# Kernel tuning notes

Measured on AMD Instinct MI355X. Metric: run time of the kernel, lower is better.

## Reference

```python
import jax, jax.numpy as jnp
import numpy as np

B, T, I, H = 128, 800, 300, 32  # batch, sl, input dim, hidden


def setup_inputs() -> dict:
    key = jax.random.key(0)
    ks = jax.random.split(key, 10)
    s_h = 1.0 / np.sqrt(H)
    s_t = 1.0 / np.sqrt(T)
    s_f = 1.0 / np.sqrt(H * T)
    u = lambda k, shape, s: jax.random.uniform(k, shape, jnp.float32, -s, s)
    return {
        "x": jax.random.normal(ks[0], (B, T, I), jnp.float32),
        "W_ih": u(ks[1], (4 * H, I), s_h),   # torch gate order: i, f, g, o
        "W_hh": u(ks[2], (4 * H, H), s_h),
        "b_ih": u(ks[3], (4 * H,), s_h),
        "b_hh": u(ks[4], (4 * H,), s_h),
        "Ww": u(ks[5], (T, T), s_t),         # Linear(sl, sl)
        "bw": u(ks[6], (T,), s_t),
        "Wfc": u(ks[7], (1, H * T), s_f),    # Linear(h*sl, 1)
        "bfc": u(ks[8], (1,), s_f),
    }


def _lstm(x, W_ih, W_hh, b_ih, b_hh):
    # Precompute input projections for all timesteps: [B, T, 4H]
    gx = jnp.einsum('bti,gi->btg', x, W_ih) + b_ih + b_hh
    h0 = jnp.zeros((x.shape[0], H), x.dtype)
    c0 = jnp.zeros_like(h0)

    def step(carry, g_t):
        h, c = carry
        g = g_t + h @ W_hh.T  # [B, 4H]
        i_g, f_g, g_g, o_g = jnp.split(g, 4, axis=-1)
        i_g = jax.nn.sigmoid(i_g)
        f_g = jax.nn.sigmoid(f_g)
        g_g = jnp.tanh(g_g)
        o_g = jax.nn.sigmoid(o_g)
        c = f_g * c + i_g * g_g
        h = o_g * jnp.tanh(c)
        return (h, c), h

    _, hs = jax.lax.scan(step, (h0, c0), jnp.swapaxes(gx, 0, 1))  # hs: [T, B, H]
    return jnp.swapaxes(hs, 0, 1)  # [B, T, H]


def reference(x, W_ih, W_hh, b_ih, b_hh, Ww, bw, Wfc, bfc):
    out = _lstm(x, W_ih, W_hh, b_ih, b_hh)  # [B, T, H]
    # permute -> Linear(sl, sl) over the seq axis -> permute back, fused in one einsum
    # q[b, s, h] = sum_t out[b, t, h] * Ww[s, t] + bw[s]
    q = jnp.einsum('bth,st->bsh', out, Ww) + bw[None, :, None]
    qk = out * q  # [B, T, H]
    out_fc = qk.reshape(qk.shape[0], -1) @ Wfc.T + bfc  # [B, 1]
    return (out_fc, qk)
```

## Files before the change

kernel.cpp:

```cpp
#include <hip/hip_runtime.h>
#include <stdint.h>

#define B_SZ 128
#define T_SZ 800
#define I_SZ 300
#define KPAD 320
#define H_SZ 32
#define G_SZ 128
#define NWIN 50
#define NBUF 4
#define TP   808
#define NTILE 50
#define NGRP 13

typedef float f32x4 __attribute__((ext_vector_type(4)));
typedef _Float16 half8 __attribute__((ext_vector_type(8)));
typedef _Float16 half2v __attribute__((ext_vector_type(2)));

union FragH { half8 v; _Float16 h[8]; uint4 u4; };
union PkU  { uint u; _Float16 h[2]; };
union HsU  { ushort s; _Float16 h; };
union Pk2  { uint u; half2v v; };

#if __has_builtin(__builtin_amdgcn_permlane32_swap)
#define HAVE_PL32 1
#else
#define HAVE_PL32 0
#endif

#if __has_builtin(__builtin_amdgcn_fdot2) && __has_builtin(__builtin_amdgcn_mov_dpp)
#define HAVE_DOT2 1
#else
#define HAVE_DOT2 0
#endif

__device__ __forceinline__ float tanhfast(float x) {
    float ax = fabsf(x);
    float z = __expf(-2.f * ax);
    float r = __fdividef(1.f - z, 1.f + z);
    return __builtin_copysignf(r, x);
}
__device__ __forceinline__ float sigmoidf_(float x) {
    return __fdividef(1.f, 1.f + __expf(-x));
}
__device__ __forceinline__ float bcast_lane(float v, int srclane) {
    return __int_as_float(__builtin_amdgcn_readlane(__float_as_int(v), srclane));
}

__global__ __launch_bounds__(256) void k_prep(
    const float* __restrict__ W_ih, const float* __restrict__ Ww,
    _Float16* __restrict__ W_ihH, _Float16* __restrict__ WwH)
{
    int i = blockIdx.x * 256 + threadIdx.x;
    if (i < G_SZ * KPAD) {
        int r = i / KPAD, k = i - r * KPAD;
        W_ihH[i] = (k < I_SZ) ? (_Float16)W_ih[r * I_SZ + k] : (_Float16)0.f;
    }
    int j = i - G_SZ * KPAD;
    if (j >= 0 && j < T_SZ * T_SZ) WwH[j] = (_Float16)Ww[j];
}

__global__ __launch_bounds__(256) void k_main(
    const float* __restrict__ x, const _Float16* __restrict__ W_ihH,
    const float* __restrict__ W_hh,
    const float* __restrict__ b_ih, const float* __restrict__ b_hh,
    const float* __restrict__ bfc,
    _Float16* __restrict__ histG,
    float* __restrict__ out)
{
    const int b    = blockIdx.x;
    const int tid  = threadIdx.x;
    const int wave = tid >> 6;
    const int lane = tid & 63;
    const int m16  = lane & 15;
    const int quad = lane >> 4;

    __shared__ __align__(16) ushort hist[H_SZ][TP];
    __shared__ __align__(16) uint   gxbuf[NBUF][16][64];
    __shared__ int produced, consumed;

    if (tid == 0) { produced = 0; consumed = 0; out[b] = bfc[0]; }
    __syncthreads();

    if (wave == 0) {
#if HAVE_PL32
        bool pl_pick_x;
        {
            auto t2 = __builtin_amdgcn_permlane32_swap(lane, lane, false, false);
            pl_pick_x = ((int)__builtin_amdgcn_readlane((int)t2[0], 63) < (int)H_SZ);
        }
#endif
        float c = 0.f;

#if HAVE_DOT2 && HAVE_PL32
        uint WpA[16], WpB[16];
#pragma unroll
        for (int j = 0; j < 16; ++j) {
            HsU a0_, a1_, b0_, b1_;
            a0_.h = (_Float16)W_hh[lane * H_SZ + 2*j];
            a1_.h = (_Float16)W_hh[lane * H_SZ + 2*j + 1];
            b0_.h = (_Float16)W_hh[(lane + 64) * H_SZ + 2*j];
            b1_.h = (_Float16)W_hh[(lane + 64) * H_SZ + 2*j + 1];
            WpA[j] = (uint)a0_.s | ((uint)a1_.s << 16);
            WpB[j] = (uint)b0_.s | ((uint)b1_.s << 16);
        }
        int hpk = 0;

        for (int w = 0; w < NWIN; ++w) {
            while (__atomic_load_n(&produced, __ATOMIC_ACQUIRE) < w + 1)
                __builtin_amdgcn_s_sleep(2);
#pragma unroll 4
            for (int tl = 0; tl < 16; ++tl) {
                const int t = w * 16 + tl;
                PkU g; g.u = gxbuf[w & (NBUF - 1)][tl][lane];
                float aA0 = 0.f, aA1 = 0.f, aB0 = 0.f, aB1 = 0.f;
#pragma unroll
                for (int j = 0; j < 16; j += 2) {
                    Pk2 h0; h0.u = (uint)__builtin_amdgcn_readlane(hpk, 32 + 2*j);
                    Pk2 h1; h1.u = (uint)__builtin_amdgcn_readlane(hpk, 32 + 2*j + 2);
                    Pk2 wa0; wa0.u = WpA[j];     Pk2 wb0; wb0.u = WpB[j];
                    Pk2 wa1; wa1.u = WpA[j + 1]; Pk2 wb1; wb1.u = WpB[j + 1];
                    aA0 = __builtin_amdgcn_fdot2(wa0.v, h0.v, aA0, false);
                    aB0 = __builtin_amdgcn_fdot2(wb0.v, h0.v, aB0, false);
                    aA1 = __builtin_amdgcn_fdot2(wa1.v, h1.v, aA1, false);
                    aB1 = __builtin_amdgcn_fdot2(wb1.v, h1.v, aB1, false);
                }
                float g0 = (aA0 + aA1) + (float)g.h[0];
                float g1 = (aB0 + aB1) + (float)g.h[1];

                float a0 = sigmoidf_(g0);
                float zz = (lane < H_SZ) ? g1 : 0.5f * g1;
                float th = tanhfast(zz);
                float a1 = (lane < H_SZ) ? th : 0.5f * th + 0.5f;

                float ig  = a0 * a1;
                auto rr = __builtin_amdgcn_permlane32_swap(
                    __float_as_int(ig), __float_as_int(ig), false, false);
                float igs = __int_as_float(pl_pick_x ? (int)rr[0] : (int)rr[1]);
                c = a0 * c + igs;
                float h = a1 * tanhfast(c);

                HsU hc; hc.h = (_Float16)h;
                uint hcu = (uint)hc.s;
                uint hnb = (uint)__builtin_amdgcn_mov_dpp((int)hcu, 0xB1, 0xF, 0xF, false);
                hpk = (int)((hnb << 16) | hcu);
                if (lane >= H_SZ)
                    hist[lane - H_SZ][t] = hc.s;
            }
            __atomic_store_n(&consumed, w + 1, __ATOMIC_RELEASE);
        }
#else
        float W0[H_SZ], W1[H_SZ];
#pragma unroll
        for (int k = 0; k < H_SZ; ++k) W0[k] = W_hh[lane * H_SZ + k];
#pragma unroll
        for (int k = 0; k < H_SZ; ++k) W1[k] = W_hh[(lane + 64) * H_SZ + k];
        float hprev = 0.f;

        for (int w = 0; w < NWIN; ++w) {
            while (__atomic_load_n(&produced, __ATOMIC_ACQUIRE) < w + 1)
                __builtin_amdgcn_s_sleep(2);
#pragma unroll 4
            for (int tl = 0; tl < 16; ++tl) {
                const int t = w * 16 + tl;
                PkU g; g.u = gxbuf[w & (NBUF - 1)][tl][lane];
                float p0=0.f,p1=0.f,p2=0.f,p3=0.f;
                float q0=0.f,q1=0.f,q2=0.f,q3=0.f;
#pragma unroll
                for (int k = 0; k < H_SZ; k += 4) {
                    float h0 = bcast_lane(hprev, H_SZ + k + 0);
                    float h1 = bcast_lane(hprev, H_SZ + k + 1);
                    float h2 = bcast_lane(hprev, H_SZ + k + 2);
                    float h3 = bcast_lane(hprev, H_SZ + k + 3);
                    p0 += W0[k+0]*h0; q0 += W1[k+0]*h0;
                    p1 += W0[k+1]*h1; q1 += W1[k+1]*h1;
                    p2 += W0[k+2]*h2; q2 += W1[k+2]*h2;
                    p3 += W0[k+3]*h3; q3 += W1[k+3]*h3;
                }
                float g0 = ((p0 + p1) + (p2 + p3)) + (float)g.h[0];
                float g1 = ((q0 + q1) + (q2 + q3)) + (float)g.h[1];

                float a0 = sigmoidf_(g0);
                float zz = (lane < H_SZ) ? g1 : 0.5f * g1;
                float th = tanhfast(zz);
                float a1 = (lane < H_SZ) ? th : 0.5f * th + 0.5f;

                float ig  = a0 * a1;
                float igs = __shfl_up(ig, 32, 64);
                c = a0 * c + igs;
                float h = a1 * tanhfast(c);
                hprev = h;
                if (lane >= H_SZ) {
                    HsU hs; hs.h = (_Float16)h;
                    hist[lane - H_SZ][t] = hs.s;
                }
            }
            __atomic_store_n(&consumed, w + 1, __ATOMIC_RELEASE);
        }
#endif
    } else {
        float bias[8];
#pragma unroll
        for (int nt = 0; nt < 8; ++nt)
            bias[nt] = b_ih[nt * 16 + m16] + b_hh[nt * 16 + m16];
        const float* xb = x + (size_t)b * T_SZ * I_SZ;

        for (int w = wave - 1; w < NWIN; w += 3) {
            const float* xrow = xb + (size_t)(w * 16 + m16) * I_SZ;
            f32x4 acc[8];
#pragma unroll
            for (int nt = 0; nt < 8; ++nt) acc[nt] = (f32x4){0.f, 0.f, 0.f, 0.f};

            for (int ks = 0; ks < 9; ++ks) {
                const int k0 = ks * 32 + quad * 8;
                f32x4 x0 = *(const f32x4*)(xrow + k0);
                f32x4 x1 = *(const f32x4*)(xrow + k0 + 4);
                FragH a;
                a.h[0] = (_Float16)x0[0]; a.h[1] = (_Float16)x0[1];
                a.h[2] = (_Float16)x0[2]; a.h[3] = (_Float16)x0[3];
                a.h[4] = (_Float16)x1[0]; a.h[5] = (_Float16)x1[1];
                a.h[6] = (_Float16)x1[2]; a.h[7] = (_Float16)x1[3];
#pragma unroll
                for (int nt = 0; nt < 8; ++nt) {
                    FragH bb;
                    bb.u4 = *(const uint4*)(W_ihH + (size_t)(nt * 16 + m16) * KPAD + k0);
                    acc[nt] = __builtin_amdgcn_mfma_f32_16x16x32_f16(a.v, bb.v, acc[nt], 0, 0, 0);
                }
            }
            {
                FragH a;
#pragma unroll
                for (int jj = 0; jj < 8; ++jj) {
                    int k = 288 + quad * 8 + jj;
                    a.h[jj] = (k < I_SZ) ? (_Float16)xrow[k] : (_Float16)0.f;
                }
#pragma unroll
                for (int nt = 0; nt < 8; ++nt) {
                    FragH bb;
                    bb.u4 = *(const uint4*)(W_ihH + (size_t)(nt * 16 + m16) * KPAD + 288 + quad * 8);
                    acc[nt] = __builtin_amdgcn_mfma_f32_16x16x32_f16(a.v, bb.v, acc[nt], 0, 0, 0);
                }
            }
            while (__atomic_load_n(&consumed, __ATOMIC_ACQUIRE) < w - (NBUF - 1))
                __builtin_amdgcn_s_sleep(8);
#pragma unroll
            for (int nt = 0; nt < 4; ++nt)
#pragma unroll
                for (int r = 0; r < 4; ++r) {
                    PkU p;
                    p.h[0] = (_Float16)(acc[nt][r]     + bias[nt]);
                    p.h[1] = (_Float16)(acc[nt + 4][r] + bias[nt + 4]);
                    gxbuf[w & (NBUF - 1)][quad * 4 + r][nt * 16 + m16] = p.u;
                }
            while (__atomic_load_n(&produced, __ATOMIC_ACQUIRE) != w)
                __builtin_amdgcn_s_sleep(8);
            __atomic_store_n(&produced, w + 1, __ATOMIC_RELEASE);
        }
    }

    __syncthreads();
    _Float16* hGb = histG + (size_t)b * H_SZ * T_SZ;
    for (int i = tid; i < H_SZ * (T_SZ / 8); i += 256) {
        int r = i / (T_SZ / 8), cc = i - r * (T_SZ / 8);
        *(uint4*)(hGb + (size_t)r * T_SZ + cc * 8) = *(const uint4*)&hist[r][cc * 8];
    }
}

__global__ __launch_bounds__(256) void k_attn(
    const _Float16* __restrict__ histG, const _Float16* __restrict__ WwH,
    const float* __restrict__ bw, const float* __restrict__ Wfc,
    float* __restrict__ out)
{
    const int b    = blockIdx.x;
    const int grp  = blockIdx.y;
    const int tid  = threadIdx.x;
    const int wave = tid >> 6;
    const int lane = tid & 63;
    const int m16  = lane & 15;
    const int quad = lane >> 4;

    __shared__ __align__(16) ushort histL[H_SZ][TP];

    const _Float16* hb = histG + (size_t)b * H_SZ * T_SZ;
    for (int i = tid; i < H_SZ * (T_SZ / 8); i += 256) {
        int r = i / (T_SZ / 8), c = i - r * (T_SZ / 8);
        *(uint4*)&histL[r][c * 8] = *(const uint4*)(hb + (size_t)r * T_SZ + c * 8);
    }
    __syncthreads();

    const int st = grp * 4 + wave;
    if (st >= NTILE) return;
    const int s0 = st * 16;

    float* region = out + B_SZ + (size_t)b * T_SZ * H_SZ;
    f32x4 acc0 = (f32x4){0.f,0.f,0.f,0.f};
    f32x4 acc1 = (f32x4){0.f,0.f,0.f,0.f};
    const _Float16* wwrow = WwH + (size_t)(s0 + m16) * T_SZ;

#pragma unroll 2
    for (int t0 = 0; t0 < T_SZ; t0 += 32) {
        FragH a, b0, b1;
        a.u4  = *(const uint4*)(wwrow + t0 + quad * 8);
        b0.u4 = *(const uint4*)&histL[m16][t0 + quad * 8];
        b1.u4 = *(const uint4*)&histL[16 + m16][t0 + quad * 8];
        acc0 = __builtin_amdgcn_mfma_f32_16x16x32_f16(a.v, b0.v, acc0, 0, 0, 0);
        acc1 = __builtin_amdgcn_mfma_f32_16x16x32_f16(a.v, b1.v, acc1, 0, 0, 0);
    }

    float fc_acc = 0.f;
#pragma unroll
    for (int r = 0; r < 4; ++r) {
        int s = s0 + quad * 4 + r;
        float bws = bw[s];
        HsU u0; u0.s = histL[m16][s];      float h0 = (float)u0.h;
        HsU u1; u1.s = histL[16 + m16][s]; float h1 = (float)u1.h;
        float q0 = acc0[r] + bws;
        float q1 = acc1[r] + bws;
        float qk0 = h0 * q0;
        float qk1 = h1 * q1;
        region[(size_t)s * H_SZ + m16]      = qk0;
        region[(size_t)s * H_SZ + 16 + m16] = qk1;
        fc_acc += qk0 * Wfc[s * H_SZ + m16];
        fc_acc += qk1 * Wfc[s * H_SZ + 16 + m16];
    }

#pragma unroll
    for (int off = 32; off > 0; off >>= 1)
        fc_acc += __shfl_down(fc_acc, off, 64);
    if (lane == 0) atomicAdd(out + b, fc_acc);
}

extern "C" void kernel_launch(void* const* d_in, const int* in_sizes, int n_in,
                              void* d_out, int out_size, void* d_ws, size_t ws_size,
                              hipStream_t stream) {
    const float* x    = (const float*)d_in[0];
    const float* W_ih = (const float*)d_in[1];
    const float* W_hh = (const float*)d_in[2];
    const float* b_ih = (const float*)d_in[3];
    const float* b_hh = (const float*)d_in[4];
    const float* Ww   = (const float*)d_in[5];
    const float* bw   = (const float*)d_in[6];
    const float* Wfc  = (const float*)d_in[7];
    const float* bfc  = (const float*)d_in[8];

    float* out = (float*)d_out;

    _Float16* W_ihH = (_Float16*)d_ws;
    _Float16* WwH   = (_Float16*)((char*)d_ws + (size_t)G_SZ * KPAD * 2);
    _Float16* histG = (_Float16*)((char*)d_ws + (size_t)G_SZ * KPAD * 2
                                             + (size_t)T_SZ * T_SZ * 2);

    int prep_n = G_SZ * KPAD + T_SZ * T_SZ;
    k_prep<<<(prep_n + 255) / 256, 256, 0, stream>>>(W_ih, Ww, W_ihH, WwH);
    k_main<<<B_SZ, 256, 0, stream>>>(x, W_ihH, W_hh, b_ih, b_hh, bfc, histG, out);
    k_attn<<<dim3(B_SZ, NGRP), 256, 0, stream>>>(histG, WwH, bw, Wfc, out);
}
```

Before: 397.1 us.

## Process two batch elements per block to interleave independent LSTM recurrences

Each k_main block now handles two batch elements, running both LSTM recurrences interleaved in the single recurrence wave and computing input projections for both in the producer waves. The intent is to hide the latency of the serial per-timestep dependency chain (dot products, lane broadcasts, activations) by giving the scheduler two independent chains. The grid is halved, so fewer CUs are used and per-block work and shared memory roughly double.

```diff
diff --git a/kernel.cpp b/kernel.cpp
--- a/kernel.cpp
+++ b/kernel.cpp
@@ -68,18 +68,20 @@
     _Float16* __restrict__ histG,
     float* __restrict__ out)
 {
-    const int b    = blockIdx.x;
+    const int bA   = blockIdx.x * 2;
+    const int bB   = bA + 1;
     const int tid  = threadIdx.x;
     const int wave = tid >> 6;
     const int lane = tid & 63;
     const int m16  = lane & 15;
     const int quad = lane >> 4;
 
-    __shared__ __align__(16) ushort hist[H_SZ][TP];
-    __shared__ __align__(16) uint   gxbuf[NBUF][16][64];
+    __shared__ __align__(16) ushort histA[H_SZ][TP];
+    __shared__ __align__(16) ushort histB[H_SZ][TP];
+    __shared__ __align__(16) uint   gxbuf[2][NBUF][16][64];
     __shared__ int produced, consumed;
 
-    if (tid == 0) { produced = 0; consumed = 0; out[b] = bfc[0]; }
+    if (tid == 0) { produced = 0; consumed = 0; out[bA] = bfc[0]; out[bB] = bfc[0]; }
     __syncthreads();
 
     if (wave == 0) {
@@ -90,7 +92,7 @@
             pl_pick_x = ((int)__builtin_amdgcn_readlane((int)t2[0], 63) < (int)H_SZ);
         }
 #endif
-        float c = 0.f;
+        float cA = 0.f, cB = 0.f;
 
 #if HAVE_DOT2 && HAVE_PL32
         uint WpA[16], WpB[16];
@@ -104,48 +106,74 @@
             WpA[j] = (uint)a0_.s | ((uint)a1_.s << 16);
             WpB[j] = (uint)b0_.s | ((uint)b1_.s << 16);
         }
-        int hpk = 0;
+        int hpkA = 0, hpkB = 0;
 
         for (int w = 0; w < NWIN; ++w) {
             while (__atomic_load_n(&produced, __ATOMIC_ACQUIRE) < w + 1)
                 __builtin_amdgcn_s_sleep(2);
+            const int wb = w & (NBUF - 1);
 #pragma unroll 4
             for (int tl = 0; tl < 16; ++tl) {
                 const int t = w * 16 + tl;
-                PkU g; g.u = gxbuf[w & (NBUF - 1)][tl][lane];
-                float aA0 = 0.f, aA1 = 0.f, aB0 = 0.f, aB1 = 0.f;
+                PkU gA; gA.u = gxbuf[0][wb][tl][lane];
+                PkU gB; gB.u = gxbuf[1][wb][tl][lane];
+                float fA0=0.f,fA1=0.f,oA0=0.f,oA1=0.f;
+                float fB0=0.f,fB1=0.f,oB0=0.f,oB1=0.f;
 #pragma unroll
                 for (int j = 0; j < 16; j += 2) {
-                    Pk2 h0; h0.u = (uint)__builtin_amdgcn_readlane(hpk, 32 + 2*j);
-                    Pk2 h1; h1.u = (uint)__builtin_amdgcn_readlane(hpk, 32 + 2*j + 2);
+                    Pk2 hA0; hA0.u = (uint)__builtin_amdgcn_readlane(hpkA, 32 + 2*j);
+                    Pk2 hB0; hB0.u = (uint)__builtin_amdgcn_readlane(hpkB, 32 + 2*j);
+                    Pk2 hA1; hA1.u = (uint)__builtin_amdgcn_readlane(hpkA, 32 + 2*j + 2);
+                    Pk2 hB1; hB1.u = (uint)__builtin_amdgcn_readlane(hpkB, 32 + 2*j + 2);
                     Pk2 wa0; wa0.u = WpA[j];     Pk2 wb0; wb0.u = WpB[j];
                     Pk2 wa1; wa1.u = WpA[j + 1]; Pk2 wb1; wb1.u = WpB[j + 1];
-                    aA0 = __builtin_amdgcn_fdot2(wa0.v, h0.v, aA0, false);
-                    aB0 = __builtin_amdgcn_fdot2(wb0.v, h0.v, aB0, false);
-                    aA1 = __builtin_amdgcn_fdot2(wa1.v, h1.v, aA1, false);
-                    aB1 = __builtin_amdgcn_fdot2(wb1.v, h1.v, aB1, false);
-                }
-                float g0 = (aA0 + aA1) + (float)g.h[0];
-                float g1 = (aB0 + aB1) + (float)g.h[1];
-
-                float a0 = sigmoidf_(g0);
-                float zz = (lane < H_SZ) ? g1 : 0.5f * g1;
-                float th = tanhfast(zz);
-                float a1 = (lane < H_SZ) ? th : 0.5f * th + 0.5f;
-
-                float ig  = a0 * a1;
-                auto rr = __builtin_amdgcn_permlane32_swap(
-                    __float_as_int(ig), __float_as_int(ig), false, false);
-                float igs = __int_as_float(pl_pick_x ? (int)rr[0] : (int)rr[1]);
-                c = a0 * c + igs;
-                float h = a1 * tanhfast(c);
-
-                HsU hc; hc.h = (_Float16)h;
-                uint hcu = (uint)hc.s;
-                uint hnb = (uint)__builtin_amdgcn_mov_dpp((int)hcu, 0xB1, 0xF, 0xF, false);
-                hpk = (int)((hnb << 16) | hcu);
-                if (lane >= H_SZ)
-                    hist[lane - H_SZ][t] = hc.s;
+                    fA0 = __builtin_amdgcn_fdot2(wa0.v, hA0.v, fA0, false);
+                    fB0 = __builtin_amdgcn_fdot2(wa0.v, hB0.v, fB0, false);
+                    oA0 = __builtin_amdgcn_fdot2(wb0.v, hA0.v, oA0, false);
+                    oB0 = __builtin_amdgcn_fdot2(wb0.v, hB0.v, oB0, false);
+                    fA1 = __builtin_amdgcn_fdot2(wa1.v, hA1.v, fA1, false);
+                    fB1 = __builtin_amdgcn_fdot2(wa1.v, hB1.v, fB1, false);
+                    oA1 = __builtin_amdgcn_fdot2(wb1.v, hA1.v, oA1, false);
+                    oB1 = __builtin_amdgcn_fdot2(wb1.v, hB1.v, oB1, false);
+                }
+                float g0A = (fA0 + fA1) + (float)gA.h[0];
+                float g0B = (fB0 + fB1) + (float)gB.h[0];
+                float g1A = (oA0 + oA1) + (float)gA.h[1];
+                float g1B = (oB0 + oB1) + (float)gB.h[1];
+
+                float a0A = sigmoidf_(g0A);
+                float a0B = sigmoidf_(g0B);
+                float zzA = (lane < H_SZ) ? g1A : 0.5f * g1A;
+                float zzB = (lane < H_SZ) ? g1B : 0.5f * g1B;
+                float thA = tanhfast(zzA);
+                float thB = tanhfast(zzB);
+                float a1A = (lane < H_SZ) ? thA : 0.5f * thA + 0.5f;
+                float a1B = (lane < H_SZ) ? thB : 0.5f * thB + 0.5f;
+
+                float igA = a0A * a1A;
+                float igB = a0B * a1B;
+                auto rrA = __builtin_amdgcn_permlane32_swap(
+                    __float_as_int(igA), __float_as_int(igA), false, false);
+                auto rrB = __builtin_amdgcn_permlane32_swap(
+                    __float_as_int(igB), __float_as_int(igB), false, false);
+                float igsA = __int_as_float(pl_pick_x ? (int)rrA[0] : (int)rrA[1]);
+                float igsB = __int_as_float(pl_pick_x ? (int)rrB[0] : (int)rrB[1]);
+                cA = a0A * cA + igsA;
+                cB = a0B * cB + igsB;
+                float hA = a1A * tanhfast(cA);
+                float hB = a1B * tanhfast(cB);
+
+                HsU hcA; hcA.h = (_Float16)hA;
+                HsU hcB; hcB.h = (_Float16)hB;
+                uint hcuA = (uint)hcA.s, hcuB = (uint)hcB.s;
+                uint hnbA = (uint)__builtin_amdgcn_mov_dpp((int)hcuA, 0xB1, 0xF, 0xF, false);
+                uint hnbB = (uint)__builtin_amdgcn_mov_dpp((int)hcuB, 0xB1, 0xF, 0xF, false);
+                hpkA = (int)((hnbA << 16) | hcuA);
+                hpkB = (int)((hnbB << 16) | hcuB);
+                if (lane >= H_SZ) {
+                    histA[lane - H_SZ][t] = hcA.s;
+                    histB[lane - H_SZ][t] = hcB.s;
+                }
             }
             __atomic_store_n(&consumed, w + 1, __ATOMIC_RELEASE);
         }
@@ -155,44 +183,48 @@
         for (int k = 0; k < H_SZ; ++k) W0[k] = W_hh[lane * H_SZ + k];
 #pragma unroll
         for (int k = 0; k < H_SZ; ++k) W1[k] = W_hh[(lane + 64) * H_SZ + k];
-        float hprev = 0.f;
+        float hpA = 0.f, hpB = 0.f;
 
         for (int w = 0; w < NWIN; ++w) {
             while (__atomic_load_n(&produced, __ATOMIC_ACQUIRE) < w + 1)
                 __builtin_amdgcn_s_sleep(2);
-#pragma unroll 4
+            const int wb = w & (NBUF - 1);
+#pragma unroll 2
             for (int tl = 0; tl < 16; ++tl) {
                 const int t = w * 16 + tl;
-                PkU g; g.u = gxbuf[w & (NBUF - 1)][tl][lane];
-                float p0=0.f,p1=0.f,p2=0.f,p3=0.f;
-                float q0=0.f,q1=0.f,q2=0.f,q3=0.f;
-#pragma unroll
-                for (int k = 0; k < H_SZ; k += 4) {
-                    float h0 = bcast_lane(hprev, H_SZ + k + 0);
-                    float h1 = bcast_lane(hprev, H_SZ + k + 1);
-                    float h2 = bcast_lane(hprev, H_SZ + k + 2);
-                    float h3 = bcast_lane(hprev, H_SZ + k + 3);
-                    p0 += W0[k+0]*h0; q0 += W1[k+0]*h0;
-                    p1 += W0[k+1]*h1; q1 += W1[k+1]*h1;
-                    p2 += W0[k+2]*h2; q2 += W1[k+2]*h2;
-                    p3 += W0[k+3]*h3; q3 += W1[k+3]*h3;
-                }
-                float g0 = ((p0 + p1) + (p2 + p3)) + (float)g.h[0];
-                float g1 = ((q0 + q1) + (q2 + q3)) + (float)g.h[1];
-
-                float a0 = sigmoidf_(g0);
-                float zz = (lane < H_SZ) ? g1 : 0.5f * g1;
-                float th = tanhfast(zz);
-                float a1 = (lane < H_SZ) ? th : 0.5f * th + 0.5f;
-
-                float ig  = a0 * a1;
-                float igs = __shfl_up(ig, 32, 64);
-                c = a0 * c + igs;
-                float h = a1 * tanhfast(c);
-                hprev = h;
-                if (lane >= H_SZ) {
-                    HsU hs; hs.h = (_Float16)h;
-                    hist[lane - H_SZ][t] = hs.s;
+                for (int sel = 0; sel < 2; ++sel) {
+                    float& c = sel ? cB : cA;
+                    float& hp = sel ? hpB : hpA;
+                    PkU g; g.u = gxbuf[sel][wb][tl][lane];
+                    float p0=0.f,p1=0.f,p2=0.f,p3=0.f;
+                    float q0=0.f,q1=0.f,q2=0.f,q3=0.f;
+#pragma unroll
+                    for (int k = 0; k < H_SZ; k += 4) {
+                        float h0 = bcast_lane(hp, H_SZ + k + 0);
+                        float h1 = bcast_lane(hp, H_SZ + k + 1);
+                        float h2 = bcast_lane(hp, H_SZ + k + 2);
+                        float h3 = bcast_lane(hp, H_SZ + k + 3);
+                        p0 += W0[k+0]*h0; q0 += W1[k+0]*h0;
+                        p1 += W0[k+1]*h1; q1 += W1[k+1]*h1;
+                        p2 += W0[k+2]*h2; q2 += W1[k+2]*h2;
+                        p3 += W0[k+3]*h3; q3 += W1[k+3]*h3;
+                    }
+                    float g0 = ((p0 + p1) + (p2 + p3)) + (float)g.h[0];
+                    float g1 = ((q0 + q1) + (q2 + q3)) + (float)g.h[1];
+                    float a0 = sigmoidf_(g0);
+                    float zz = (lane < H_SZ) ? g1 : 0.5f * g1;
+                    float th = tanhfast(zz);
+                    float a1 = (lane < H_SZ) ? th : 0.5f * th + 0.5f;
+                    float ig  = a0 * a1;
+                    float igs = __shfl_up(ig, 32, 64);
+                    c = a0 * c + igs;
+                    float h = a1 * tanhfast(c);
+                    hp = h;
+                    if (lane >= H_SZ) {
+                        HsU hs; hs.h = (_Float16)h;
+                        if (sel) histB[lane - H_SZ][t] = hs.s;
+                        else     histA[lane - H_SZ][t] = hs.s;
+                    }
                 }
             }
             __atomic_store_n(&consumed, w + 1, __ATOMIC_RELEASE);
@@ -203,14 +235,12 @@
 #pragma unroll
         for (int nt = 0; nt < 8; ++nt)
             bias[nt] = b_ih[nt * 16 + m16] + b_hh[nt * 16 + m16];
-        const float* xb = x + (size_t)b * T_SZ * I_SZ;
-
-        for (int w = wave - 1; w < NWIN; w += 3) {
-            const float* xrow = xb + (size_t)(w * 16 + m16) * I_SZ;
-            f32x4 acc[8];
+        const float* xbA = x + (size_t)bA * T_SZ * I_SZ;
+        const float* xbB = x + (size_t)bB * T_SZ * I_SZ;
+
+        auto gxcompute = [&](const float* xrow, f32x4 (&acc)[8]) {
 #pragma unroll
             for (int nt = 0; nt < 8; ++nt) acc[nt] = (f32x4){0.f, 0.f, 0.f, 0.f};
-
             for (int ks = 0; ks < 9; ++ks) {
                 const int k0 = ks * 32 + quad * 8;
                 f32x4 x0 = *(const f32x4*)(xrow + k0);
@@ -241,8 +271,8 @@
                     acc[nt] = __builtin_amdgcn_mfma_f32_16x16x32_f16(a.v, bb.v, acc[nt], 0, 0, 0);
                 }
             }
-            while (__atomic_load_n(&consumed, __ATOMIC_ACQUIRE) < w - (NBUF - 1))
-                __builtin_amdgcn_s_sleep(8);
+        };
+        auto gxstore = [&](int sel, int wb, f32x4 (&acc)[8]) {
 #pragma unroll
             for (int nt = 0; nt < 4; ++nt)
 #pragma unroll
@@ -250,8 +280,20 @@
                     PkU p;
                     p.h[0] = (_Float16)(acc[nt][r]     + bias[nt]);
                     p.h[1] = (_Float16)(acc[nt + 4][r] + bias[nt + 4]);
-                    gxbuf[w & (NBUF - 1)][quad * 4 + r][nt * 16 + m16] = p.u;
-                }
+                    gxbuf[sel][wb][quad * 4 + r][nt * 16 + m16] = p.u;
+                }
+        };
+
+        for (int w = wave - 1; w < NWIN; w += 3) {
+            const int wb = w & (NBUF - 1);
+            const size_t roff = (size_t)(w * 16 + m16) * I_SZ;
+            f32x4 acc[8];
+            gxcompute(xbA + roff, acc);
+            while (__atomic_load_n(&consumed, __ATOMIC_ACQUIRE) < w - (NBUF - 1))
+                __builtin_amdgcn_s_sleep(8);
+            gxstore(0, wb, acc);
+            gxcompute(xbB + roff, acc);
+            gxstore(1, wb, acc);
             while (__atomic_load_n(&produced, __ATOMIC_ACQUIRE) != w)
                 __builtin_amdgcn_s_sleep(8);
             __atomic_store_n(&produced, w + 1, __ATOMIC_RELEASE);
@@ -259,10 +301,12 @@
     }
 
     __syncthreads();
-    _Float16* hGb = histG + (size_t)b * H_SZ * T_SZ;
+    _Float16* hGA = histG + (size_t)bA * H_SZ * T_SZ;
+    _Float16* hGB = histG + (size_t)bB * H_SZ * T_SZ;
     for (int i = tid; i < H_SZ * (T_SZ / 8); i += 256) {
         int r = i / (T_SZ / 8), cc = i - r * (T_SZ / 8);
-        *(uint4*)(hGb + (size_t)r * T_SZ + cc * 8) = *(const uint4*)&hist[r][cc * 8];
+        *(uint4*)(hGA + (size_t)r * T_SZ + cc * 8) = *(const uint4*)&histA[r][cc * 8];
+        *(uint4*)(hGB + (size_t)r * T_SZ + cc * 8) = *(const uint4*)&histB[r][cc * 8];
     }
 }
 
@@ -352,6 +396,6 @@
 
     int prep_n = G_SZ * KPAD + T_SZ * T_SZ;
     k_prep<<<(prep_n + 255) / 256, 256, 0, stream>>>(W_ih, Ww, W_ihH, WwH);
-    k_main<<<B_SZ, 256, 0, stream>>>(x, W_ihH, W_hh, b_ih, b_hh, bfc, histG, out);
+    k_main<<<B_SZ / 2, 256, 0, stream>>>(x, W_ihH, W_hh, b_ih, b_hh, bfc, histG, out);
     k_attn<<<dim3(B_SZ, NGRP), 256, 0, stream>>>(histG, WwH, bw, Wfc, out);
 }
```

Measured after the change: 575.2 us. 1.45x slower.
